# Kernel optimization log

Measured on AMD Instinct MI355X. Metric: run time of the kernel, lower is better.

Reference implementation:

```python
import jax, jax.numpy as jnp
import numpy as np

D_MODEL = 768
N_HEADS = 8
HEAD_DIM = D_MODEL // N_HEADS
B, S, A = 8, 8192, 512


def setup_inputs() -> dict:
    key = jax.random.key(0)
    ks = jax.random.split(key, 12)
    hidden_states = jax.random.normal(ks[0], (B, S, D_MODEL), dtype=jnp.float32)
    # unique anchors per batch element (scatter with duplicates is ill-defined)
    anchor_indices = jax.vmap(lambda k: jax.random.permutation(k, S)[:A])(
        jax.random.split(ks[1], B)).astype(jnp.int64)
    std = 1.0 / np.sqrt(D_MODEL)
    def lin(kw, kb):
        w = jax.random.uniform(kw, (D_MODEL, D_MODEL), jnp.float32, -std, std)
        b = jax.random.uniform(kb, (D_MODEL,), jnp.float32, -std, std)
        return w, b
    wq, bq = lin(ks[2], ks[3])
    wk, bk = lin(ks[4], ks[5])
    wv, bv = lin(ks[6], ks[7])
    wo, bo = lin(ks[8], ks[9])
    ln_g = jnp.ones((D_MODEL,), jnp.float32)
    ln_b = jnp.zeros((D_MODEL,), jnp.float32)
    return dict(hidden_states=hidden_states, anchor_indices=anchor_indices,
                ln_g=ln_g, ln_b=ln_b, wq=wq, bq=bq, wk=wk, bk=bk,
                wv=wv, bv=bv, wo=wo, bo=bo)


def reference(hidden_states, anchor_indices, ln_g, ln_b, wq, bq, wk, bk, wv, bv, wo, bo):
    batch, seq_len, d_model = hidden_states.shape
    n_anchors = anchor_indices.shape[1]
    # gather anchor tokens: (B, A, D)
    anchor_hidden = jnp.take_along_axis(hidden_states, anchor_indices[..., None], axis=1)
    # LayerNorm (eps=1e-5, matching nn.LayerNorm default)
    mu = jnp.mean(anchor_hidden, axis=-1, keepdims=True)
    var = jnp.var(anchor_hidden, axis=-1, keepdims=True)
    x = (anchor_hidden - mu) * jax.lax.rsqrt(var + 1e-5) * ln_g + ln_b
    # QKV projections -> (B, H, A, Hd)
    def heads(y):
        return y.reshape(batch, n_anchors, N_HEADS, HEAD_DIM).transpose(0, 2, 1, 3)
    q = heads(x @ wq.T + bq)
    k = heads(x @ wk.T + bk)
    v = heads(x @ wv.T + bv)
    scale = 1.0 / np.sqrt(HEAD_DIM)
    scores = jnp.einsum('bhad,bhed->bhae', q, k) * scale  # (B,H,A,A)
    attn = jax.nn.softmax(scores, axis=-1)  # dropout is identity in eval
    out = jnp.einsum('bhae,bhed->bhad', attn, v)
    out = out.transpose(0, 2, 1, 3).reshape(batch, n_anchors, d_model)
    out = out @ wo.T + bo
    # scatter back into zeros at anchor positions
    batch_idx = jnp.arange(batch)[:, None]
    output = jnp.zeros_like(hidden_states).at[batch_idx, anchor_indices].set(out)
    return output
```

## Files before the change

kernel.cpp:

```cpp
#include <hip/hip_runtime.h>

#define DM 768
#define NHEAD 8
#define HDIM 96
#define NB 8
#define SEQ 8192
#define NA 512
#define MROW (NB*NA)
#define NQKV (3*DM)
#define QBLK 32
#define ATTNB 1024
#define AFILLB 512
#define GFILLB 512
#define PFILLB 256

typedef __attribute__((ext_vector_type(4))) float f32x4;
typedef __attribute__((ext_vector_type(8))) short s16x8;

static __device__ __forceinline__ unsigned short f2bf(float x) {
  unsigned int u = __float_as_uint(x);
  u += 0x7fffu + ((u >> 16) & 1u);
  return (unsigned short)(u >> 16);
}

static __device__ __forceinline__ void gld_lds16(const void* g, void* l) {
  __builtin_amdgcn_global_load_lds(
      (const __attribute__((address_space(1))) unsigned int*)g,
      (__attribute__((address_space(3))) unsigned int*)l, 16, 0, 0);
}

__global__ __launch_bounds__(512) void prologue(
    const float* __restrict__ hs, const int* __restrict__ anc,
    const float* __restrict__ gam, const float* __restrict__ bet,
    const float* __restrict__ wq, const float* __restrict__ wk,
    const float* __restrict__ wv, const float* __restrict__ wo,
    unsigned short* __restrict__ xh,
    unsigned short* __restrict__ w1h, unsigned short* __restrict__ woh,
    f32x4* __restrict__ fillp, int fstart, int fend)
{
  const int bid = blockIdx.x;
  const int t = threadIdx.x;
  if (bid < 512) {
    const int w = t >> 6, lane = t & 63;
    const int r = bid * 8 + w;
    const int b = r >> 9, a = r & (NA - 1);
    const int idx = anc[b * NA + a];
    const float4* src4 = reinterpret_cast<const float4*>(hs + ((size_t)b * SEQ + idx) * DM);
    float4 e[3];
    float s = 0.f, ss = 0.f;
    #pragma unroll
    for (int p = 0; p < 3; ++p) {
      e[p] = src4[lane * 3 + p];
      s  += e[p].x + e[p].y + e[p].z + e[p].w;
      ss += e[p].x*e[p].x + e[p].y*e[p].y + e[p].z*e[p].z + e[p].w*e[p].w;
    }
    #pragma unroll
    for (int o = 1; o < 64; o <<= 1) { s += __shfl_xor(s, o); ss += __shfl_xor(ss, o); }
    const float mu = s * (1.f / DM);
    const float var = ss * (1.f / DM) - mu * mu;
    const float rstd = rsqrtf(var + 1e-5f);
    uint2* dst = reinterpret_cast<uint2*>(xh + (size_t)r * DM);
    const float4* g4 = reinterpret_cast<const float4*>(gam);
    const float4* b4 = reinterpret_cast<const float4*>(bet);
    #pragma unroll
    for (int p = 0; p < 3; ++p) {
      const float4 gv = g4[lane * 3 + p], bv = b4[lane * 3 + p];
      const float y0 = (e[p].x - mu) * rstd * gv.x + bv.x;
      const float y1 = (e[p].y - mu) * rstd * gv.y + bv.y;
      const float y2 = (e[p].z - mu) * rstd * gv.z + bv.z;
      const float y3 = (e[p].w - mu) * rstd * gv.w + bv.w;
      uint2 pk;
      pk.x = (unsigned)f2bf(y0) | ((unsigned)f2bf(y1) << 16);
      pk.y = (unsigned)f2bf(y2) | ((unsigned)f2bf(y3) << 16);
      dst[lane * 3 + p] = pk;
    }
  } else if (bid < 800) {
    const int base = (bid - 512) * 2048;
    const int T1_4 = (NQKV * DM) / 4;
    const int TW_4 = (DM * DM) / 4;
    #pragma unroll
    for (int rep = 0; rep < 4; ++rep) {
      const int i = base + rep * 512 + t;
      float4 v; unsigned short* dh; int e4;
      if (i < T1_4) {
        v = (i < TW_4) ? reinterpret_cast<const float4*>(wq)[i]
          : (i < 2*TW_4) ? reinterpret_cast<const float4*>(wk)[i - TW_4]
                         : reinterpret_cast<const float4*>(wv)[i - 2*TW_4];
        dh = w1h; e4 = i;
      } else {
        const int j = i - T1_4;
        v = reinterpret_cast<const float4*>(wo)[j];
        dh = woh; e4 = j;
      }
      uint2 ph;
      ph.x = (unsigned)f2bf(v.x) | ((unsigned)f2bf(v.y) << 16);
      ph.y = (unsigned)f2bf(v.z) | ((unsigned)f2bf(v.w) << 16);
      reinterpret_cast<uint2*>(dh)[e4] = ph;
    }
  } else {
    const f32x4 z = {0.f, 0.f, 0.f, 0.f};
    int i = fstart + (bid - 800) * 512 + t;
    for (; i < fend; i += PFILLB * 512) __builtin_nontemporal_store(z, fillp + i);
  }
}

template<int EPI, int BM, int BN, int NCOMP, int GCOLS>
__global__ __launch_bounds__(256, 4) void gemm_t(
    const unsigned short* __restrict__ Ah,
    const unsigned short* __restrict__ Bh,
    const float* __restrict__ biasq, const float* __restrict__ biask, const float* __restrict__ biasv,
    unsigned short* __restrict__ qh,
    unsigned short* __restrict__ kh,
    unsigned short* __restrict__ vh,
    const float* __restrict__ biaso, const int* __restrict__ anc,
    float* __restrict__ outp,
    f32x4* __restrict__ fillp, int fstart, int fend, int nfillb)
{
  constexpr int MI = BM / 32, NJ = BN / 32;
  __shared__ unsigned short sA[BM * 64], sB[BN * 64];
  const int bidx = blockIdx.x;
  if (bidx >= NCOMP) {
    const f32x4 z = {0.f, 0.f, 0.f, 0.f};
    int i = fstart + (bidx - NCOMP) * 256 + threadIdx.x;
    for (; i < fend; i += nfillb * 256) __builtin_nontemporal_store(z, fillp + i);
    return;
  }
  const int tid = threadIdx.x, lane = tid & 63, w = tid >> 6;
  const int wr = w >> 1, wc = w & 1;
  const unsigned int wg = ((unsigned)bidx & 7) * (NCOMP >> 3) + ((unsigned)bidx >> 3);
  const int m0 = (int)(wg / GCOLS) * BM, n0 = (int)(wg % GCOLS) * BN;
  const int rsel = lane & 15, kg = lane >> 4;
  f32x4 acc[MI][NJ] = {};

  for (int k0 = 0; k0 < DM; k0 += 64) {
    __syncthreads();
    #pragma unroll
    for (int c = 0; c < (BM + BN) / 32; ++c) {
      const int gg = c * 256 + w * 64;
      const int g = gg + lane;
      if (g < BM * 8) {
        const int row = g >> 3, slot = g & 7;
        const int kk = k0 + ((slot ^ (row & 7)) << 3);
        gld_lds16(Ah + (size_t)(m0 + row) * DM + kk, sA + gg * 8);
      } else {
        const int g2 = g - BM * 8;
        const int row = g2 >> 3, slot = g2 & 7;
        const int kk = k0 + ((slot ^ (row & 7)) << 3);
        gld_lds16(Bh + (size_t)(n0 + row) * DM + kk, sB + (gg - BM * 8) * 8);
      }
    }
    __syncthreads();
    #pragma unroll
    for (int s = 0; s < 2; ++s) {
      s16x8 af[MI], bf[NJ];
      #pragma unroll
      for (int i = 0; i < MI; ++i) {
        const int row = wr * (MI * 16) + i * 16 + rsel;
        const int as = (((s << 2) | kg) ^ (row & 7));
        af[i] = *reinterpret_cast<const s16x8*>(sA + row * 64 + as * 8);
      }
      #pragma unroll
      for (int j = 0; j < NJ; ++j) {
        const int col = wc * (NJ * 16) + j * 16 + rsel;
        const int bs = (((s << 2) | kg) ^ (col & 7));
        bf[j] = *reinterpret_cast<const s16x8*>(sB + col * 64 + bs * 8);
      }
      #pragma unroll
      for (int i = 0; i < MI; ++i)
        #pragma unroll
        for (int j = 0; j < NJ; ++j)
          acc[i][j] = __builtin_amdgcn_mfma_f32_16x16x32_bf16(af[i], bf[j], acc[i][j], 0, 0, 0);
    }
  }

  #pragma unroll
  for (int i = 0; i < MI; ++i)
    #pragma unroll
    for (int j = 0; j < NJ; ++j)
      #pragma unroll
      for (int r = 0; r < 4; ++r) {
        const int row = m0 + wr * (MI * 16) + i * 16 + kg * 4 + r;
        const int col = n0 + wc * (NJ * 16) + j * 16 + rsel;
        const float v = acc[i][j][r];
        const int b = row >> 9, a = row & (NA - 1);
        if (EPI == 1) {
          const int sec = (col >= 2 * DM) ? 2 : (col >= DM ? 1 : 0);
          const int f = col - sec * DM;
          const int hh = f / HDIM, d = f - hh * HDIM;
          const float* bp = (sec == 0) ? biasq : (sec == 1) ? biask : biasv;
          const float val = v + bp[f];
          const int bhh = b * NHEAD + hh;
          if (sec == 0) {
            const size_t o = ((size_t)bhh * NA + a) * HDIM + d; qh[o] = f2bf(val);
          } else if (sec == 1) {
            const size_t o = ((size_t)bhh * NA + a) * HDIM + d; kh[o] = f2bf(val);
          } else {
            const size_t o = ((size_t)bhh * HDIM + d) * NA + a; vh[o] = f2bf(val);
          }
        } else {
          const int sidx = anc[b * NA + a];
          outp[((size_t)b * SEQ + sidx) * DM + col] = v + biaso[col];
        }
      }
}

__global__ __launch_bounds__(512, 4) void attn_fused(
    const unsigned short* __restrict__ qh,
    const unsigned short* __restrict__ kh,
    const unsigned short* __restrict__ vh,
    unsigned short* __restrict__ oh,
    f32x4* __restrict__ fillp, int fstart, int fend)
{
  __shared__ unsigned int S[QBLK * 512];
  __shared__ float rsum_lds[QBLK];
  if (blockIdx.x >= ATTNB) {
    const f32x4 z = {0.f, 0.f, 0.f, 0.f};
    int i = fstart + (blockIdx.x - ATTNB) * 512 + threadIdx.x;
    for (; i < fend; i += AFILLB * 512) __builtin_nontemporal_store(z, fillp + i);
    return;
  }
  const int blk = blockIdx.x;
  const int xcd = blk & 7, slot = blk >> 3;
  const int qt = slot & 15, bh = (slot >> 4) * 8 + xcd;
  const int b = bh >> 3, h = bh & 7;
  const int tid = threadIdx.x, lane = tid & 63, w = tid >> 6;
  const int rt = w & 1, ctq = w >> 1;
  const int rsel = lane & 15, kg = lane >> 4;
  const int q0 = qt * QBLK;

  s16x8 qf[3];
  {
    const size_t qrow = (size_t)bh * NA + q0 + rt * 16 + rsel;
    const unsigned short* qp = qh + qrow * HDIM + kg * 8;
    #pragma unroll
    for (int kc = 0; kc < 3; ++kc)
      qf[kc] = *reinterpret_cast<const s16x8*>(qp + kc * 32);
  }
  const float scale = 0.10206207261596575f;
  const unsigned short* kb_h = kh + (size_t)bh * NA * HDIM + (size_t)rsel * HDIM + kg * 8;

  #pragma unroll
  for (int ct2 = 0; ct2 < 8; ++ct2) {
    const int ct = ctq * 8 + ct2;
    f32x4 acc = {0.f, 0.f, 0.f, 0.f};
    const unsigned short* kp = kb_h + (size_t)(ct * 16) * HDIM;
    s16x8 kf0 = *reinterpret_cast<const s16x8*>(kp);
    s16x8 kf1 = *reinterpret_cast<const s16x8*>(kp + 32);
    s16x8 kf2 = *reinterpret_cast<const s16x8*>(kp + 64);
    acc = __builtin_amdgcn_mfma_f32_16x16x32_bf16(qf[0], kf0, acc, 0, 0, 0);
    acc = __builtin_amdgcn_mfma_f32_16x16x32_bf16(qf[1], kf1, acc, 0, 0, 0);
    acc = __builtin_amdgcn_mfma_f32_16x16x32_bf16(qf[2], kf2, acc, 0, 0, 0);
    #pragma unroll
    for (int r = 0; r < 4; ++r) {
      int row = rt * 16 + kg * 4 + r;
      int col = ct * 16 + rsel;
      S[row * 512 + (col ^ ((row & 7) << 2))] = __float_as_uint(acc[r] * scale);
    }
  }
  __syncthreads();

  {
    const int row = w * 4 + (lane >> 4);
    const int sub = lane & 15;
    const int srow = (row & 7) << 2;
    unsigned int* rowp = &S[row * 512];
    float sum = 0.f;
    #pragma unroll
    for (int i = 0; i < 8; ++i) {
      int c = sub * 4 + i * 64;
      uint4 u = *reinterpret_cast<const uint4*>(rowp + (c ^ srow));
      float p0 = __expf(__uint_as_float(u.x));
      float p1 = __expf(__uint_as_float(u.y));
      float p2 = __expf(__uint_as_float(u.z));
      float p3 = __expf(__uint_as_float(u.w));
      sum += p0 + p1 + p2 + p3;
      uint4 pk;
      pk.x = ((unsigned)f2bf(p0)) << 16;
      pk.y = ((unsigned)f2bf(p1)) << 16;
      pk.z = ((unsigned)f2bf(p2)) << 16;
      pk.w = ((unsigned)f2bf(p3)) << 16;
      *reinterpret_cast<uint4*>(rowp + (c ^ srow)) = pk;
    }
    sum += __shfl_xor(sum, 1);
    sum += __shfl_xor(sum, 2);
    sum += __shfl_xor(sum, 4);
    sum += __shfl_xor(sum, 8);
    if (sub == 0) rsum_lds[row] = 1.f / sum;
  }
  __syncthreads();

  const unsigned short* vb_h = vh + (size_t)bh * HDIM * NA + (size_t)rsel * NA + kg * 8;
  for (int task = w; task < 12; task += 8) {
    const int nt = task % 6, rt2 = task / 6;
    f32x4 acc = {0.f, 0.f, 0.f, 0.f};
    const int row = rt2 * 16 + rsel;
    const int srow = (row & 7) << 2;
    const unsigned int* rowp = &S[row * 512];
    const unsigned short* vp = vb_h + (size_t)(nt * 16) * NA;
    #pragma unroll
    for (int kc = 0; kc < 16; ++kc) {
      int c = kc * 32 + kg * 8;
      s16x8 vfh = *reinterpret_cast<const s16x8*>(vp + kc * 32);
      uint4 ua = *reinterpret_cast<const uint4*>(rowp + ((c) ^ srow));
      uint4 ub = *reinterpret_cast<const uint4*>(rowp + ((c + 4) ^ srow));
      s16x8 ph;
      ph[0] = (short)(ua.x >> 16); ph[1] = (short)(ua.y >> 16);
      ph[2] = (short)(ua.z >> 16); ph[3] = (short)(ua.w >> 16);
      ph[4] = (short)(ub.x >> 16); ph[5] = (short)(ub.y >> 16);
      ph[6] = (short)(ub.z >> 16); ph[7] = (short)(ub.w >> 16);
      acc = __builtin_amdgcn_mfma_f32_16x16x32_bf16(ph, vfh, acc, 0, 0, 0);
    }
    #pragma unroll
    for (int r = 0; r < 4; ++r) {
      const float rinv = rsum_lds[rt2 * 16 + kg * 4 + r];
      const int rowg = b * NA + q0 + rt2 * 16 + kg * 4 + r;
      size_t o = (size_t)rowg * DM + h * HDIM + nt * 16 + rsel;
      oh[o] = f2bf(acc[r] * rinv);
    }
  }
}

extern "C" void kernel_launch(void* const* d_in, const int* in_sizes, int n_in,
                              void* d_out, int out_size, void* d_ws, size_t ws_size,
                              hipStream_t stream)
{
  const float* hs   = (const float*)d_in[0];
  const int*   anc  = (const int*)d_in[1];
  const float* ln_g = (const float*)d_in[2];
  const float* ln_b = (const float*)d_in[3];
  const float* wq = (const float*)d_in[4];
  const float* bq = (const float*)d_in[5];
  const float* wk = (const float*)d_in[6];
  const float* bk = (const float*)d_in[7];
  const float* wv = (const float*)d_in[8];
  const float* bv = (const float*)d_in[9];
  const float* wo = (const float*)d_in[10];
  const float* bo = (const float*)d_in[11];
  float* outp = (float*)d_out;

  char* ws = (char*)d_ws;
  size_t off = 0;
  auto take = [&](size_t bytes) { char* p = ws + off; off += (bytes + 255) & ~(size_t)255; return p; };
  unsigned short* xh  = (unsigned short*)take((size_t)MROW * DM * 2);
  unsigned short* w1h = (unsigned short*)take((size_t)NQKV * DM * 2);
  unsigned short* woh = (unsigned short*)take((size_t)DM * DM * 2);
  const size_t qkvsz = (size_t)NB * NHEAD * NA * HDIM * 2;
  unsigned short* qhb = (unsigned short*)take(qkvsz);
  unsigned short* khb = (unsigned short*)take(qkvsz);
  unsigned short* vhb = (unsigned short*)take(qkvsz);
  unsigned short* ohb = (unsigned short*)take((size_t)MROW * DM * 2);

  const int n4 = out_size / 4;
  const int f1 = n4 / 4;
  const int f2 = (int)(((long long)n4 * 5) / 8);

  prologue<<<800 + PFILLB, 512, 0, stream>>>(
      hs, anc, ln_g, ln_b, wq, wk, wv, wo, xh, w1h, woh,
      (f32x4*)outp, 0, f1);
  gemm_t<1, 128, 96, 768, 24><<<768 + GFILLB, 256, 0, stream>>>(
      xh, w1h, bq, bk, bv, qhb, khb, vhb,
      nullptr, nullptr, nullptr,
      (f32x4*)outp, f1, f2, GFILLB);
  attn_fused<<<ATTNB + AFILLB, 512, 0, stream>>>(
      qhb, khb, vhb, ohb, (f32x4*)outp, f2, n4);
  gemm_t<2, 64, 96, 512, 8><<<512, 256, 0, stream>>>(
      ohb, woh, nullptr, nullptr, nullptr,
      nullptr, nullptr, nullptr,
      bo, anc, outp,
      nullptr, 0, 0, 1);
}
```

Before: 107.6 us.

## Move zero-fill out of prologue and interleave fill blocks with QKV GEMM blocks

Removes the output zero-fill from the prologue kernel, so the prologue now does only the gather/LayerNorm and weight conversion. The fill work is split between the QKV GEMM and the attention kernel, with the split point moved so the GEMM covers the first 11/20 of the output. Inside the GEMM grid, fill blocks are interleaved with compute blocks (3 compute to 2 fill in every 5 block IDs) instead of being appended at the end. The aim is to overlap the memory-bound fill with the compute-bound GEMM across CUs. The added modulo index mapping changes block scheduling order and may disturb the GEMM's L2 grouping.

```diff
diff --git a/kernel.cpp b/kernel.cpp
--- a/kernel.cpp
+++ b/kernel.cpp
@@ -12,7 +12,6 @@
 #define ATTNB 1024
 #define AFILLB 512
 #define GFILLB 512
-#define PFILLB 256
 
 typedef __attribute__((ext_vector_type(4))) float f32x4;
 typedef __attribute__((ext_vector_type(8))) short s16x8;
@@ -35,8 +34,7 @@
     const float* __restrict__ wq, const float* __restrict__ wk,
     const float* __restrict__ wv, const float* __restrict__ wo,
     unsigned short* __restrict__ xh,
-    unsigned short* __restrict__ w1h, unsigned short* __restrict__ woh,
-    f32x4* __restrict__ fillp, int fstart, int fend)
+    unsigned short* __restrict__ w1h, unsigned short* __restrict__ woh)
 {
   const int bid = blockIdx.x;
   const int t = threadIdx.x;
@@ -74,7 +72,7 @@
       pk.y = (unsigned)f2bf(y2) | ((unsigned)f2bf(y3) << 16);
       dst[lane * 3 + p] = pk;
     }
-  } else if (bid < 800) {
+  } else {
     const int base = (bid - 512) * 2048;
     const int T1_4 = (NQKV * DM) / 4;
     const int TW_4 = (DM * DM) / 4;
@@ -97,14 +95,10 @@
       ph.y = (unsigned)f2bf(v.z) | ((unsigned)f2bf(v.w) << 16);
       reinterpret_cast<uint2*>(dh)[e4] = ph;
     }
-  } else {
-    const f32x4 z = {0.f, 0.f, 0.f, 0.f};
-    int i = fstart + (bid - 800) * 512 + t;
-    for (; i < fend; i += PFILLB * 512) __builtin_nontemporal_store(z, fillp + i);
-  }
-}
-
-template<int EPI, int BM, int BN, int NCOMP, int GCOLS>
+  }
+}
+
+template<int EPI, int BM, int BN, int NCOMP, int GCOLS, int ILV>
 __global__ __launch_bounds__(256, 4) void gemm_t(
     const unsigned short* __restrict__ Ah,
     const unsigned short* __restrict__ Bh,
@@ -114,20 +108,27 @@
     unsigned short* __restrict__ vh,
     const float* __restrict__ biaso, const int* __restrict__ anc,
     float* __restrict__ outp,
-    f32x4* __restrict__ fillp, int fstart, int fend, int nfillb)
+    f32x4* __restrict__ fillp, int fstart, int fend)
 {
   constexpr int MI = BM / 32, NJ = BN / 32;
   __shared__ unsigned short sA[BM * 64], sB[BN * 64];
   const int bidx = blockIdx.x;
-  if (bidx >= NCOMP) {
-    const f32x4 z = {0.f, 0.f, 0.f, 0.f};
-    int i = fstart + (bidx - NCOMP) * 256 + threadIdx.x;
-    for (; i < fend; i += nfillb * 256) __builtin_nontemporal_store(z, fillp + i);
-    return;
+  int cidx;
+  if (ILV) {
+    const int m = bidx % 5;
+    if (m >= 3) {
+      const f32x4 z = {0.f, 0.f, 0.f, 0.f};
+      int i = fstart + ((bidx / 5) * 2 + (m - 3)) * 256 + threadIdx.x;
+      for (; i < fend; i += GFILLB * 256) __builtin_nontemporal_store(z, fillp + i);
+      return;
+    }
+    cidx = (bidx / 5) * 3 + m;
+  } else {
+    cidx = bidx;
   }
   const int tid = threadIdx.x, lane = tid & 63, w = tid >> 6;
   const int wr = w >> 1, wc = w & 1;
-  const unsigned int wg = ((unsigned)bidx & 7) * (NCOMP >> 3) + ((unsigned)bidx >> 3);
+  const unsigned int wg = ((unsigned)cidx & 7) * (NCOMP >> 3) + ((unsigned)cidx >> 3);
   const int m0 = (int)(wg / GCOLS) * BM, n0 = (int)(wg % GCOLS) * BN;
   const int rsel = lane & 15, kg = lane >> 4;
   f32x4 acc[MI][NJ] = {};
@@ -351,21 +352,19 @@
   unsigned short* ohb = (unsigned short*)take((size_t)MROW * DM * 2);
 
   const int n4 = out_size / 4;
-  const int f1 = n4 / 4;
-  const int f2 = (int)(((long long)n4 * 5) / 8);
-
-  prologue<<<800 + PFILLB, 512, 0, stream>>>(
-      hs, anc, ln_g, ln_b, wq, wk, wv, wo, xh, w1h, woh,
-      (f32x4*)outp, 0, f1);
-  gemm_t<1, 128, 96, 768, 24><<<768 + GFILLB, 256, 0, stream>>>(
+  const int f2 = (int)(((long long)n4 * 11) / 20);
+
+  prologue<<<800, 512, 0, stream>>>(
+      hs, anc, ln_g, ln_b, wq, wk, wv, wo, xh, w1h, woh);
+  gemm_t<1, 128, 96, 768, 24, 1><<<1280, 256, 0, stream>>>(
       xh, w1h, bq, bk, bv, qhb, khb, vhb,
       nullptr, nullptr, nullptr,
-      (f32x4*)outp, f1, f2, GFILLB);
+      (f32x4*)outp, 0, f2);
   attn_fused<<<ATTNB + AFILLB, 512, 0, stream>>>(
       qhb, khb, vhb, ohb, (f32x4*)outp, f2, n4);
-  gemm_t<2, 64, 96, 512, 8><<<512, 256, 0, stream>>>(
+  gemm_t<2, 64, 96, 512, 8, 0><<<512, 256, 0, stream>>>(
       ohb, woh, nullptr, nullptr, nullptr,
       nullptr, nullptr, nullptr,
       bo, anc, outp,
-      nullptr, 0, 0, 1);
-}
+      nullptr, 0, 0);
+}
```

After: 125.6 us. 1.17x slower.
